# Optimization experiments

Hardware: AMD Instinct MI355X
Metric: run time of the kernel (lower is better)

## Reference

```python
import jax, jax.numpy as jnp
import numpy as np

N_SESS = 4096
N_TRIALS = 2048


def setup_inputs() -> dict:
    key = jax.random.key(0)
    k1, k2 = jax.random.split(key)
    # chose_left is a one-hot choice; chose_right = 1 - chose_left; outcome in {0,1}
    chose_left = jax.random.bernoulli(k1, 0.5, (N_SESS, N_TRIALS)).astype(jnp.float32)
    chose_right = 1.0 - chose_left
    outcome = jax.random.bernoulli(k2, 0.5, (N_SESS, N_TRIALS)).astype(jnp.float32)
    inp = jnp.stack([chose_left, chose_right, outcome], axis=-1)  # (n_sess, n_trials, 3)
    # raw logits; AlphaParam applies sigmoid. logit(0.8), logit(0.6)
    p_stay_raw = jnp.array([np.log(0.8 / 0.2)], dtype=jnp.float32)
    c_raw = jnp.array([np.log(0.6 / 0.4)], dtype=jnp.float32)
    return {"input": inp, "p_stay_raw": p_stay_raw, "c_raw": c_raw}


def _forward(inp, p_stay_raw, c_raw):
    p = jax.nn.sigmoid(p_stay_raw)[0]
    c = jax.nn.sigmoid(c_raw)[0]
    # With complement_c_rew=complement_c_diff=True, all four c params equal c.
    # ev_mat (4,2): rows = [left&rew, left&unrew, right&rew, right&unrew]
    col0 = 0.5 * jnp.stack([1 + c, 1 - c, 1 - c, 1 + c])
    col1 = 0.5 * jnp.stack([1 - c, 1 + c, 1 + c, 1 - c])
    ev_mat = jnp.stack([col0, col1], axis=1)  # (4, 2)
    trans_mat = 0.5 * jnp.stack([jnp.stack([1 + p, 1 - p]),
                                 jnp.stack([1 - p, 1 + p])])  # (2, 2)

    n_sess = inp.shape[0]
    init_state = jnp.full((n_sess, 2), 0.5, dtype=inp.dtype)

    def step(state, x):  # state: (n_sess, 2), x: (n_sess, 3)
        cl, cr, o = x[:, 0], x[:, 1], x[:, 2]
        sel = jnp.stack([cl * o, cl * (1 - o), cr * o, cr * (1 - o)], axis=1)  # (n_sess, 4)
        evidence = sel @ ev_mat            # (n_sess, 2)
        like = evidence * state            # (n_sess, 2)
        like_sum = like.sum(axis=1)        # (n_sess,)
        zero = like_sum == 0
        like = jnp.where(zero[:, None], state, like)
        like_sum = jnp.where(zero, 1.0, like_sum)
        norm_like = like / like_sum[:, None]
        new_state = norm_like @ trans_mat  # (n_sess, 2)
        return new_state, new_state

    # scan over trials (time axis); output stacked as (n_trials, n_sess, 2)
    _, out = jax.lax.scan(step, init_state, jnp.swapaxes(inp, 0, 1))
    return jnp.swapaxes(out, 0, 1)  # (n_sess, n_trials, 2)


def reference(input, p_stay_raw, c_raw):
    return _forward(input, p_stay_raw, c_raw)
```

## Files before the change

### kernel.cpp

```cpp
#include <hip/hip_runtime.h>


constexpr int NSESS   = 4096;
constexpr int NTRIALS = 2048;
constexpr int WAVES   = 4;
constexpr int THREADS = WAVES * 64;
constexpr int TPW     = NTRIALS / WAVES;
constexpr int LCH     = TPW / 64;

__device__ __forceinline__ float frcp(float x) {
    return __builtin_amdgcn_rcpf(x);
}

__global__ __launch_bounds__(THREADS) void hmm_kernel(
    const float* __restrict__ inp,
    const float* __restrict__ p_raw,
    const float* __restrict__ c_raw,
    float* __restrict__ out)
{
    __shared__ float lds_tot[WAVES][4];

    const int t    = threadIdx.x;
    const int lane = t & 63;
    const int w    = t >> 6;
    const int sess = blockIdx.x;

    const float p = 1.0f / (1.0f + __expf(-p_raw[0]));
    const float c = 1.0f / (1.0f + __expf(-c_raw[0]));
    const float A = 0.5f * (1.0f + c), B = 0.5f * (1.0f - c);
    const float q = 0.5f * (1.0f + p), r = 0.5f * (1.0f - p);

    const float4* xv = reinterpret_cast<const float4*>(inp)
                     + (size_t)sess * (NTRIALS * 3 / 4)
                     + w * (TPW * 3 / 4) + lane * (LCH * 3 / 4);
    const float4 v0 = xv[0], v1 = xv[1], v2 = xv[2];
    const float4 v3 = xv[3], v4 = xv[4], v5 = xv[5];

    float p00 = 1.f, p01 = 0.f, p10 = 0.f, p11 = 1.f;
    float e0_0, e0_1, e0_2, e0_3, e0_4, e0_5, e0_6, e0_7;
    float e1_0, e1_1, e1_2, e1_3, e1_4, e1_5, e1_6, e1_7;

#define TRIAL(CL, CR, O, E0, E1)                                        \
    {                                                                   \
        float d0_ = (CL) * (O) + (CR) * (1.f - (O));                    \
        float d1_ = (CL) * (1.f - (O)) + (CR) * (O);                    \
        E0 = d0_ * A + d1_ * B;                                         \
        E1 = d0_ * B + d1_ * A;                                         \
        float m00_, m01_, m10_, m11_;                                   \
        if (E0 == 0.f && E1 == 0.f) { m00_ = q; m01_ = r; m10_ = r; m11_ = q; } \
        else { m00_ = E0 * q; m01_ = E0 * r; m10_ = E1 * r; m11_ = E1 * q; } \
        float n00_ = p00 * m00_ + p01 * m10_;                           \
        float n01_ = p00 * m01_ + p01 * m11_;                           \
        float n10_ = p10 * m00_ + p11 * m10_;                           \
        float n11_ = p10 * m01_ + p11 * m11_;                           \
        p00 = n00_; p01 = n01_; p10 = n10_; p11 = n11_;                 \
    }

    TRIAL(v0.x, v0.y, v0.z, e0_0, e1_0)
    TRIAL(v0.w, v1.x, v1.y, e0_1, e1_1)
    TRIAL(v1.z, v1.w, v2.x, e0_2, e1_2)
    TRIAL(v2.y, v2.z, v2.w, e0_3, e1_3)
    TRIAL(v3.x, v3.y, v3.z, e0_4, e1_4)
    TRIAL(v3.w, v4.x, v4.y, e0_5, e1_5)
    TRIAL(v4.z, v4.w, v5.x, e0_6, e1_6)
    TRIAL(v5.y, v5.z, v5.w, e0_7, e1_7)
#undef TRIAL

    {
        float inv = frcp(p00 + p01 + p10 + p11);
        p00 *= inv; p01 *= inv; p10 *= inv; p11 *= inv;
    }

#define SCAN(D)                                                         \
    {                                                                   \
        float a00_ = __shfl_up(p00, D);                                 \
        float a01_ = __shfl_up(p01, D);                                 \
        float a10_ = __shfl_up(p10, D);                                 \
        float a11_ = (1.f - a00_) - (a01_ + a10_);                      \
        if (lane >= D) {                                                \
            float n00_ = a00_ * p00 + a01_ * p10;                       \
            float n01_ = a00_ * p01 + a01_ * p11;                       \
            float n10_ = a10_ * p00 + a11_ * p10;                       \
            float n11_ = a10_ * p01 + a11_ * p11;                       \
            float inv_ = frcp(n00_ + n01_ + n10_ + n11_);               \
            p00 = n00_ * inv_; p01 = n01_ * inv_;                       \
            p10 = n10_ * inv_; p11 = n11_ * inv_;                       \
        }                                                               \
    }

    SCAN(1) SCAN(2) SCAN(4) SCAN(8) SCAN(16) SCAN(32)
#undef SCAN

    if (lane == 63) {
        lds_tot[w][0] = p00; lds_tot[w][1] = p01;
        lds_tot[w][2] = p10; lds_tot[w][3] = p11;
    }
    __syncthreads();

    float s0 = 0.5f, s1 = 0.5f;
    for (int ww = 0; ww < w; ++ww) {
        float t00 = lds_tot[ww][0], t01 = lds_tot[ww][1];
        float t10 = lds_tot[ww][2], t11 = lds_tot[ww][3];
        float n0 = s0 * t00 + s1 * t10;
        float n1 = s0 * t01 + s1 * t11;
        float inv = frcp(n0 + n1);
        s0 = n0 * inv; s1 = n1 * inv;
    }
    float c00 = __shfl_up(p00, 1);
    float c01 = __shfl_up(p01, 1);
    float c10 = __shfl_up(p10, 1);
    float c11 = (1.f - c00) - (c01 + c10);
    float u0 = s0, u1 = s1;
    if (lane > 0) {
        float n0 = s0 * c00 + s1 * c10;
        float n1 = s0 * c01 + s1 * c11;
        float inv = frcp(n0 + n1);
        u0 = n0 * inv; u1 = n1 * inv;
    }

#define REPLAY(E0, E1, O0, O1)                                          \
    {                                                                   \
        float w0_ = u0 * (E0), w1_ = u1 * (E1);                         \
        if (w0_ + w1_ == 0.f) { w0_ = u0; w1_ = u1; }                   \
        float n0_ = w0_ * q + w1_ * r;                                  \
        float n1_ = w0_ * r + w1_ * q;                                  \
        float inv_ = frcp(n0_ + n1_);         \
        O0 = n0_ * inv_; O1 = n1_ * inv_;                               \
        u0 = n0_; u1 = n1_;                                             \
    }

    float4* yv = reinterpret_cast<float4*>(out)
               + (size_t)sess * (NTRIALS * 2 / 4) + w * (TPW * 2 / 4) + lane * 4;

    float o0a, o1a, o0b, o1b;
    REPLAY(e0_0, e1_0, o0a, o1a)
    REPLAY(e0_1, e1_1, o0b, o1b)
    yv[0] = make_float4(o0a, o1a, o0b, o1b);
    REPLAY(e0_2, e1_2, o0a, o1a)
    REPLAY(e0_3, e1_3, o0b, o1b)
    yv[1] = make_float4(o0a, o1a, o0b, o1b);
    REPLAY(e0_4, e1_4, o0a, o1a)
    REPLAY(e0_5, e1_5, o0b, o1b)
    yv[2] = make_float4(o0a, o1a, o0b, o1b);
    REPLAY(e0_6, e1_6, o0a, o1a)
    REPLAY(e0_7, e1_7, o0b, o1b)
    yv[3] = make_float4(o0a, o1a, o0b, o1b);
#undef REPLAY
}

extern "C" void kernel_launch(void* const* d_in, const int* in_sizes, int n_in,
                              void* d_out, int out_size, void* d_ws, size_t ws_size,
                              hipStream_t stream) {
    const float* inp   = (const float*)d_in[0];
    const float* p_raw = (const float*)d_in[1];
    const float* c_raw = (const float*)d_in[2];
    float* out = (float*)d_out;

    hmm_kernel<<<dim3(NSESS), dim3(THREADS), 0, stream>>>(inp, p_raw, c_raw, out);
}
```

Measured before the change: 170.6 us.

## Split HMM scan into two kernels with bit-packed evidence and workspace handoff

The single fused kernel becomes two. The first computes per-chunk transition products and packs each chunk's evidence into a bitmask, with a prefix state, in a workspace. The second replays the chunk from those bits and writes the outputs. The evidence computation is reduced to a bit test (cl==o), dropping the zero-likelihood branch and the (1-a) reconstruction. This lowers register pressure and per-kernel arithmetic, at the cost of an extra launch and workspace traffic. It assumes one-hot inputs and nonzero c.

```diff
diff --git a/kernel.cpp b/kernel.cpp
--- a/kernel.cpp
+++ b/kernel.cpp
@@ -7,16 +7,17 @@
 constexpr int THREADS = WAVES * 64;
 constexpr int TPW     = NTRIALS / WAVES;
 constexpr int LCH     = TPW / 64;
+constexpr int CPS     = NTRIALS / LCH;
 
 __device__ __forceinline__ float frcp(float x) {
     return __builtin_amdgcn_rcpf(x);
 }
 
-__global__ __launch_bounds__(THREADS) void hmm_kernel(
+__global__ __launch_bounds__(THREADS) void hmm_pass1(
     const float* __restrict__ inp,
     const float* __restrict__ p_raw,
     const float* __restrict__ c_raw,
-    float* __restrict__ out)
+    uint4* __restrict__ ws)
 {
     __shared__ float lds_tot[WAVES][4];
 
@@ -27,7 +28,8 @@
 
     const float p = 1.0f / (1.0f + __expf(-p_raw[0]));
     const float c = 1.0f / (1.0f + __expf(-c_raw[0]));
-    const float A = 0.5f * (1.0f + c), B = 0.5f * (1.0f - c);
+    const float A = 0.5f * (1.0f + c);
+    const float B = 0.5f * (1.0f - c);
     const float q = 0.5f * (1.0f + p), r = 0.5f * (1.0f - p);
 
     const float4* xv = reinterpret_cast<const float4*>(inp)
@@ -36,35 +38,33 @@
     const float4 v0 = xv[0], v1 = xv[1], v2 = xv[2];
     const float4 v3 = xv[3], v4 = xv[4], v5 = xv[5];
 
+    unsigned bits = 0u;
     float p00 = 1.f, p01 = 0.f, p10 = 0.f, p11 = 1.f;
-    float e0_0, e0_1, e0_2, e0_3, e0_4, e0_5, e0_6, e0_7;
-    float e1_0, e1_1, e1_2, e1_3, e1_4, e1_5, e1_6, e1_7;
 
-#define TRIAL(CL, CR, O, E0, E1)                                        \
+#define STEP(CL, O, I)                                                  \
     {                                                                   \
-        float d0_ = (CL) * (O) + (CR) * (1.f - (O));                    \
-        float d1_ = (CL) * (1.f - (O)) + (CR) * (O);                    \
-        E0 = d0_ * A + d1_ * B;                                         \
-        E1 = d0_ * B + d1_ * A;                                         \
-        float m00_, m01_, m10_, m11_;                                   \
-        if (E0 == 0.f && E1 == 0.f) { m00_ = q; m01_ = r; m10_ = r; m11_ = q; } \
-        else { m00_ = E0 * q; m01_ = E0 * r; m10_ = E1 * r; m11_ = E1 * q; } \
-        float n00_ = p00 * m00_ + p01 * m10_;                           \
-        float n01_ = p00 * m01_ + p01 * m11_;                           \
-        float n10_ = p10 * m00_ + p11 * m10_;                           \
-        float n11_ = p10 * m01_ + p11 * m11_;                           \
+        const bool b_ = ((CL) == (O));           \
+        bits |= (unsigned)b_ << (I);                                    \
+        const float e0_ = b_ ? A : B;                                   \
+        const float e1_ = 1.f - e0_;                                    \
+        const float m00_ = e0_ * q, m01_ = e0_ * r;                     \
+        const float m10_ = e1_ * r, m11_ = e1_ * q;                     \
+        const float n00_ = p00 * m00_ + p01 * m10_;                     \
+        const float n01_ = p00 * m01_ + p01 * m11_;                     \
+        const float n10_ = p10 * m00_ + p11 * m10_;                     \
+        const float n11_ = p10 * m01_ + p11 * m11_;                     \
         p00 = n00_; p01 = n01_; p10 = n10_; p11 = n11_;                 \
     }
 
-    TRIAL(v0.x, v0.y, v0.z, e0_0, e1_0)
-    TRIAL(v0.w, v1.x, v1.y, e0_1, e1_1)
-    TRIAL(v1.z, v1.w, v2.x, e0_2, e1_2)
-    TRIAL(v2.y, v2.z, v2.w, e0_3, e1_3)
-    TRIAL(v3.x, v3.y, v3.z, e0_4, e1_4)
-    TRIAL(v3.w, v4.x, v4.y, e0_5, e1_5)
-    TRIAL(v4.z, v4.w, v5.x, e0_6, e1_6)
-    TRIAL(v5.y, v5.z, v5.w, e0_7, e1_7)
-#undef TRIAL
+    STEP(v0.x, v0.z, 0)
+    STEP(v0.w, v1.y, 1)
+    STEP(v1.z, v2.x, 2)
+    STEP(v2.y, v2.w, 3)
+    STEP(v3.x, v3.z, 4)
+    STEP(v3.w, v4.y, 5)
+    STEP(v4.z, v5.x, 6)
+    STEP(v5.y, v5.w, 7)
+#undef STEP
 
     {
         float inv = frcp(p00 + p01 + p10 + p11);
@@ -76,8 +76,8 @@
         float a00_ = __shfl_up(p00, D);                                 \
         float a01_ = __shfl_up(p01, D);                                 \
         float a10_ = __shfl_up(p10, D);                                 \
-        float a11_ = (1.f - a00_) - (a01_ + a10_);                      \
-        if (lane >= D) {                                                \
+        float a11_ = __shfl_up(p11, D);                                 \
+        if (lane >= (D)) {                                              \
             float n00_ = a00_ * p00 + a01_ * p10;                       \
             float n01_ = a00_ * p01 + a01_ * p11;                       \
             float n10_ = a10_ * p00 + a11_ * p10;                       \
@@ -95,6 +95,12 @@
         lds_tot[w][0] = p00; lds_tot[w][1] = p01;
         lds_tot[w][2] = p10; lds_tot[w][3] = p11;
     }
+
+    const float c00 = __shfl_up(p00, 1);
+    const float c01 = __shfl_up(p01, 1);
+    const float c10 = __shfl_up(p10, 1);
+    const float c11 = __shfl_up(p11, 1);
+
     __syncthreads();
 
     float s0 = 0.5f, s1 = 0.5f;
@@ -106,10 +112,6 @@
         float inv = frcp(n0 + n1);
         s0 = n0 * inv; s1 = n1 * inv;
     }
-    float c00 = __shfl_up(p00, 1);
-    float c01 = __shfl_up(p01, 1);
-    float c10 = __shfl_up(p10, 1);
-    float c11 = (1.f - c00) - (c01 + c10);
     float u0 = s0, u1 = s1;
     if (lane > 0) {
         float n0 = s0 * c00 + s1 * c10;
@@ -118,32 +120,60 @@
         u0 = n0 * inv; u1 = n1 * inv;
     }
 
-#define REPLAY(E0, E1, O0, O1)                                          \
+    ws[(size_t)sess * CPS + w * 64 + lane] =
+        make_uint4(bits, __float_as_uint(u0), __float_as_uint(u1), 0u);
+}
+
+__global__ __launch_bounds__(256) void hmm_pass2(
+    const uint4* __restrict__ ws,
+    const float* __restrict__ p_raw,
+    const float* __restrict__ c_raw,
+    float* __restrict__ out)
+{
+    const int g = blockIdx.x * 256 + threadIdx.x;
+
+    const float p = 1.0f / (1.0f + __expf(-p_raw[0]));
+    const float c = 1.0f / (1.0f + __expf(-c_raw[0]));
+    const float A = 0.5f * (1.0f + c);
+    const float B = 0.5f * (1.0f - c);
+    const float q = 0.5f * (1.0f + p), r = 0.5f * (1.0f - p);
+
+    const uint4 d = ws[g];
+    const unsigned bits = d.x;
+    float u0 = __uint_as_float(d.y);
+    float u1 = __uint_as_float(d.z);
+
+    const int sess  = g >> 8;
+    const int cidx  = g & (CPS - 1);
+    const int trial0 = (cidx >> 6) * TPW + (cidx & 63) * LCH;
+
+    float4* yv = reinterpret_cast<float4*>(out)
+               + ((size_t)sess * NTRIALS + trial0) / 2;
+
+#define REPLAY(I, O0, O1)                                               \
     {                                                                   \
-        float w0_ = u0 * (E0), w1_ = u1 * (E1);                         \
-        if (w0_ + w1_ == 0.f) { w0_ = u0; w1_ = u1; }                   \
-        float n0_ = w0_ * q + w1_ * r;                                  \
-        float n1_ = w0_ * r + w1_ * q;                                  \
-        float inv_ = frcp(n0_ + n1_);         \
+        const float e0_ = ((bits >> (I)) & 1u) ? A : B;                 \
+        const float e1_ = 1.f - e0_;                                    \
+        const float w0_ = u0 * e0_, w1_ = u1 * e1_;                     \
+        const float n0_ = w0_ * q + w1_ * r;                            \
+        const float n1_ = w0_ * r + w1_ * q;                            \
+        const float inv_ = frcp(n0_ + n1_);    \
         O0 = n0_ * inv_; O1 = n1_ * inv_;                               \
-        u0 = n0_; u1 = n1_;                                             \
+        u0 = n0_; u1 = n1_;    \
     }
 
-    float4* yv = reinterpret_cast<float4*>(out)
-               + (size_t)sess * (NTRIALS * 2 / 4) + w * (TPW * 2 / 4) + lane * 4;
-
     float o0a, o1a, o0b, o1b;
-    REPLAY(e0_0, e1_0, o0a, o1a)
-    REPLAY(e0_1, e1_1, o0b, o1b)
+    REPLAY(0, o0a, o1a)
+    REPLAY(1, o0b, o1b)
     yv[0] = make_float4(o0a, o1a, o0b, o1b);
-    REPLAY(e0_2, e1_2, o0a, o1a)
-    REPLAY(e0_3, e1_3, o0b, o1b)
+    REPLAY(2, o0a, o1a)
+    REPLAY(3, o0b, o1b)
     yv[1] = make_float4(o0a, o1a, o0b, o1b);
-    REPLAY(e0_4, e1_4, o0a, o1a)
-    REPLAY(e0_5, e1_5, o0b, o1b)
+    REPLAY(4, o0a, o1a)
+    REPLAY(5, o0b, o1b)
     yv[2] = make_float4(o0a, o1a, o0b, o1b);
-    REPLAY(e0_6, e1_6, o0a, o1a)
-    REPLAY(e0_7, e1_7, o0b, o1b)
+    REPLAY(6, o0a, o1a)
+    REPLAY(7, o0b, o1b)
     yv[3] = make_float4(o0a, o1a, o0b, o1b);
 #undef REPLAY
 }
@@ -155,6 +185,8 @@
     const float* p_raw = (const float*)d_in[1];
     const float* c_raw = (const float*)d_in[2];
     float* out = (float*)d_out;
+    uint4* ws  = (uint4*)d_ws;
 
-    hmm_kernel<<<dim3(NSESS), dim3(THREADS), 0, stream>>>(inp, p_raw, c_raw, out);
+    hmm_pass1<<<dim3(NSESS), dim3(THREADS), 0, stream>>>(inp, p_raw, c_raw, ws);
+    hmm_pass2<<<dim3(NSESS * CPS / 256), dim3(256), 0, stream>>>(ws, p_raw, c_raw, out);
 }
```

Measured after the change: 181.8 us. 6.6% more time.
